# Kernel tuning notes

Measured on AMD Instinct MI355X. Metric: run time of the kernel, lower is better.

Reference implementation:

```python
import jax, jax.numpy as jnp
import numpy as np

N_NODES = 100000
N_EDGES = 1600000


def _spmm(row, col, val, x, n):
    # out[i] = sum_{e: row[e]==i} val[e] * x[col[e]]  (sparse adj @ dense x)
    return jax.ops.segment_sum(val[:, None] * x[col], row, num_segments=n)


def setup_inputs() -> dict:
    key = jax.random.key(0)
    ks = jax.random.split(key, 6)
    x = jax.random.normal(ks[0], (N_NODES, 128), dtype=jnp.float32)
    edge_row = jnp.sort(jax.random.randint(ks[1], (N_EDGES,), 0, N_NODES, dtype=jnp.int64))
    edge_col = jax.random.randint(ks[2], (N_EDGES,), 0, N_NODES, dtype=jnp.int64)
    # glorot-initialized linear layers (pyg Linear with weight_initializer='glorot')
    W0 = jax.random.normal(ks[3], (128, 128), dtype=jnp.float32) * np.sqrt(2.0 / (128 + 128))
    b0 = jnp.zeros((128,), dtype=jnp.float32)
    W1 = jax.random.normal(ks[4], (128, 64), dtype=jnp.float32) * np.sqrt(2.0 / (128 + 64))
    b1 = jnp.zeros((64,), dtype=jnp.float32)
    return {"x": x, "edge_row": edge_row, "edge_col": edge_col,
            "W0": W0, "b0": b0, "W1": W1, "b1": b1}


def reference(x, edge_row, edge_col, W0, b0, W1, b1):
    n = x.shape[0]
    # adj_norm: symmetric GCN normalization D^{-1/2} A D^{-1/2}
    ones = jnp.ones(edge_row.shape[0], dtype=x.dtype)
    deg = jax.ops.segment_sum(ones, edge_row, num_segments=n)
    dinv = jnp.where(deg > 0, jax.lax.rsqrt(jnp.maximum(deg, 1.0)), 0.0).astype(x.dtype)
    val = dinv[edge_row] * dinv[edge_col]
    # layer 0: linear -> SpMM -> relu (dropout is a no-op in inference/eval)
    h = x @ W0 + b0
    h = _spmm(edge_row, edge_col, val, h, n)
    h = jax.nn.relu(h)
    # layer 1: linear -> SpMM
    h = h @ W1 + b1
    h = _spmm(edge_row, edge_col, val, h, n)
    return jax.nn.log_softmax(h, axis=-1)
```

## Files before the change

kernel.cpp:

```cpp
#include <hip/hip_runtime.h>
#include <hip/hip_bf16.h>

#define NN 100000
#define NE 1600000

typedef __bf16 bf16x8 __attribute__((ext_vector_type(8)));
typedef float  f32x4  __attribute__((ext_vector_type(4)));

__global__ __launch_bounds__(256) void build_rowptr(const int* __restrict__ row,
                                                    int* __restrict__ row_ptr,
                                                    int E, int N) {
    int e = blockIdx.x * blockDim.x + threadIdx.x;
    if (e >= E) return;
    int r  = row[e];
    int rp = (e == 0) ? -1 : row[e - 1];
    for (int i = rp + 1; i <= r; ++i) row_ptr[i] = e;
    if (e == E - 1) {
        for (int i = r + 1; i <= N; ++i) row_ptr[i] = E;
    }
}

__global__ __launch_bounds__(256) void compute_dinv(const int* __restrict__ row_ptr,
                                                    float* __restrict__ dinv, int N) {
    int i = blockIdx.x * blockDim.x + threadIdx.x;
    if (i >= N) return;
    int deg = row_ptr[i + 1] - row_ptr[i];
    dinv[i] = (deg > 0) ? rsqrtf((float)deg) : 0.0f;
}

__global__ __launch_bounds__(256) void pack_weights(const float* __restrict__ W0,
                                                    const float* __restrict__ W1,
                                                    __hip_bfloat16* __restrict__ Wt0,
                                                    __hip_bfloat16* __restrict__ Wt1) {
    int idx = blockIdx.x * 256 + threadIdx.x;
    if (idx < 128 * 128) {
        int n = idx >> 7, k = idx & 127;
        Wt0[idx] = __float2bfloat16(W0[(size_t)k * 128 + n]);
    } else if (idx < 128 * 128 + 64 * 128) {
        int r = idx - 128 * 128;
        int n = r >> 7, k = r & 127;
        Wt1[r] = __float2bfloat16(W1[(size_t)k * 64 + n]);
    }
}

template <int NO, typename InT>
__global__ __launch_bounds__(512) void gemm_mfma(const InT* __restrict__ X,
                                                 const __hip_bfloat16* __restrict__ Wt,
                                                 const float* __restrict__ bias,
                                                 const float* __restrict__ rowscale,
                                                 __hip_bfloat16* __restrict__ out, int M) {
    constexpr int NT = NO / 16;
    __shared__ unsigned short As[128 * 128];
    __shared__ unsigned short Ws[NO * 128];

    const int t = threadIdx.x;
    const int w = t >> 6, lane = t & 63;
    const int l15 = lane & 15, quad = lane >> 4;
    const int rbase = blockIdx.x * 128;

    for (int i = t; i < NO * 16; i += 512) {
        int n = i >> 4, g = i & 15;
        *(uint4*)&Ws[n * 128 + ((g ^ (n & 7)) << 3)] = ((const uint4*)Wt)[i];
    }
    if constexpr (sizeof(InT) == 4) {
        for (int i = t; i < 4096; i += 512) {
            int r = i >> 5, c2 = i & 31;
            float4 xv = make_float4(0.f, 0.f, 0.f, 0.f);
            if (rbase + r < M) xv = ((const float4*)X)[(size_t)rbase * 32 + i];
            union { __hip_bfloat162 h; unsigned int u; } p0, p1;
            p0.h = __float22bfloat162_rn(make_float2(xv.x, xv.y));
            p1.h = __float22bfloat162_rn(make_float2(xv.z, xv.w));
            int phys = ((c2 >> 1) ^ (r & 7));
            *(uint2*)&As[r * 128 + (phys << 3) + ((c2 & 1) << 2)] = make_uint2(p0.u, p1.u);
        }
    } else {
        for (int i = t; i < 2048; i += 512) {
            int r = i >> 4, g = i & 15;
            uint4 v = make_uint4(0u, 0u, 0u, 0u);
            if (rbase + r < M) v = ((const uint4*)X)[(size_t)rbase * 16 + i];
            *(uint4*)&As[r * 128 + ((g ^ (r & 7)) << 3)] = v;
        }
    }
    __syncthreads();

    f32x4 acc[NT];
#pragma unroll
    for (int nt = 0; nt < NT; ++nt) {
        float bv = bias[nt * 16 + l15];
        acc[nt][0] = bv; acc[nt][1] = bv; acc[nt][2] = bv; acc[nt][3] = bv;
    }

    const int arow = w * 16 + l15;
    const int asw  = arow & 7;
#pragma unroll
    for (int kc = 0; kc < 4; ++kc) {
        bf16x8 af = *(const bf16x8*)&As[arow * 128 + (((kc * 4 + quad) ^ asw) << 3)];
#pragma unroll
        for (int nt = 0; nt < NT; ++nt) {
            int brow = nt * 16 + l15;
            bf16x8 bfr = *(const bf16x8*)&Ws[brow * 128 + (((kc * 4 + quad) ^ (brow & 7)) << 3)];
            acc[nt] = __builtin_amdgcn_mfma_f32_16x16x32_bf16(af, bfr, acc[nt], 0, 0, 0);
        }
    }

    __hip_bfloat16* Cs = (__hip_bfloat16*)As;
#pragma unroll
    for (int r4 = 0; r4 < 4; ++r4) {
        int lrow = w * 16 + quad * 4 + r4;
        int grow = rbase + lrow;
        float sc = (grow < M) ? rowscale[grow] : 0.f;
#pragma unroll
        for (int nt = 0; nt < NT; ++nt) {
            int ct = nt * 16 + l15;
            Cs[lrow * 128 + ((((ct >> 3) ^ (lrow & 7)) << 3)) + (ct & 7)] =
                __float2bfloat16(acc[nt][r4] * sc);
        }
    }
    constexpr int RJ  = NO / 8;
    constexpr int CNT = (16 * RJ) / 64;
#pragma unroll
    for (int k = 0; k < CNT; ++k) {
        int idx = k * 64 + lane;
        int lr16 = idx / RJ, j = idx % RJ;
        int lrow = w * 16 + lr16;
        int grow = rbase + lrow;
        if (grow < M) {
            uint4 v = *(const uint4*)&Cs[lrow * 128 + ((j ^ (lrow & 7)) << 3)];
            *(uint4*)&out[(size_t)grow * NO + (j << 3)] = v;
        }
    }
}

__global__ __launch_bounds__(256) void spmm_relu_128(const int* __restrict__ row_ptr,
                                                     const int* __restrict__ col,
                                                     const float* __restrict__ dinv,
                                                     const unsigned int* __restrict__ H,
                                                     __hip_bfloat16* __restrict__ out, int N) {
    const int lane = threadIdx.x & 63;
    int i = __builtin_amdgcn_readfirstlane(blockIdx.x * 4 + (threadIdx.x >> 6));
    if (i >= N) return;
    const float di = dinv[i];
    const int e0 = __builtin_amdgcn_readfirstlane(row_ptr[i]);
    const int e1 = __builtin_amdgcn_readfirstlane(row_ptr[i + 1]);
    float accx = 0.f, accy = 0.f;
    int e = e0;
    for (; e + 16 <= e1; e += 16) {
        unsigned int u[16];
#pragma unroll
        for (int j = 0; j < 16; ++j) {
            int c = __builtin_amdgcn_readfirstlane(col[e + j]);
            u[j] = H[(size_t)c * 64 + lane];
        }
#pragma unroll
        for (int j = 0; j < 16; ++j) {
            accx += __uint_as_float(u[j] << 16);
            accy += __uint_as_float(u[j] & 0xffff0000u);
        }
    }
    for (; e + 8 <= e1; e += 8) {
        unsigned int u[8];
#pragma unroll
        for (int j = 0; j < 8; ++j) {
            int c = __builtin_amdgcn_readfirstlane(col[e + j]);
            u[j] = H[(size_t)c * 64 + lane];
        }
#pragma unroll
        for (int j = 0; j < 8; ++j) {
            accx += __uint_as_float(u[j] << 16);
            accy += __uint_as_float(u[j] & 0xffff0000u);
        }
    }
    for (; e < e1; ++e) {
        int c = __builtin_amdgcn_readfirstlane(col[e]);
        unsigned int u = H[(size_t)c * 64 + lane];
        accx += __uint_as_float(u << 16);
        accy += __uint_as_float(u & 0xffff0000u);
    }
    accx = fmaxf(accx * di, 0.f);
    accy = fmaxf(accy * di, 0.f);
    *(__hip_bfloat162*)&out[(size_t)i * 128 + 2 * lane] =
        __float22bfloat162_rn(make_float2(accx, accy));
}

__global__ __launch_bounds__(256) void spmm_logsoftmax_64(const int* __restrict__ row_ptr,
                                                          const int* __restrict__ col,
                                                          const float* __restrict__ dinv,
                                                          const unsigned short* __restrict__ H,
                                                          float* __restrict__ out, int N) {
    const int lane = threadIdx.x & 63;
    int i = __builtin_amdgcn_readfirstlane(blockIdx.x * 4 + (threadIdx.x >> 6));
    if (i >= N) return;
    const float di = dinv[i];
    const int e0 = __builtin_amdgcn_readfirstlane(row_ptr[i]);
    const int e1 = __builtin_amdgcn_readfirstlane(row_ptr[i + 1]);
    float acc = 0.f;
    int e = e0;
    for (; e + 16 <= e1; e += 16) {
        unsigned short u[16];
#pragma unroll
        for (int j = 0; j < 16; ++j) {
            int c = __builtin_amdgcn_readfirstlane(col[e + j]);
            u[j] = H[(size_t)c * 64 + lane];
        }
#pragma unroll
        for (int j = 0; j < 16; ++j)
            acc += __uint_as_float((unsigned int)u[j] << 16);
    }
    for (; e + 8 <= e1; e += 8) {
        unsigned short u[8];
#pragma unroll
        for (int j = 0; j < 8; ++j) {
            int c = __builtin_amdgcn_readfirstlane(col[e + j]);
            u[j] = H[(size_t)c * 64 + lane];
        }
#pragma unroll
        for (int j = 0; j < 8; ++j)
            acc += __uint_as_float((unsigned int)u[j] << 16);
    }
    for (; e < e1; ++e) {
        int c = __builtin_amdgcn_readfirstlane(col[e]);
        acc += __uint_as_float((unsigned int)H[(size_t)c * 64 + lane] << 16);
    }
    acc *= di;
    float m = acc;
#pragma unroll
    for (int off = 32; off > 0; off >>= 1)
        m = fmaxf(m, __shfl_xor(m, off, 64));
    float ex = __expf(acc - m);
    float s = ex;
#pragma unroll
    for (int off = 32; off > 0; off >>= 1)
        s += __shfl_xor(s, off, 64);
    out[(size_t)i * 64 + lane] = acc - m - __logf(s);
}

extern "C" void kernel_launch(void* const* d_in, const int* in_sizes, int n_in,
                              void* d_out, int out_size, void* d_ws, size_t ws_size,
                              hipStream_t stream) {
    const float* x    = (const float*)d_in[0];
    const int*   erow = (const int*)d_in[1];
    const int*   ecol = (const int*)d_in[2];
    const float* W0   = (const float*)d_in[3];
    const float* b0   = (const float*)d_in[4];
    const float* W1   = (const float*)d_in[5];
    const float* b1   = (const float*)d_in[6];
    float* out = (float*)d_out;

    char* ws = (char*)d_ws;
    int*             row_ptr = (int*)ws;
    float*           dinv    = (float*)(ws + (512u << 10));
    __hip_bfloat16*  h0b     = (__hip_bfloat16*)(ws + (1u << 20));
    __hip_bfloat16*  h1b     = (__hip_bfloat16*)(ws + 27000000u);
    __hip_bfloat16*  h2b     = (__hip_bfloat16*)(ws + 53000000u);
    __hip_bfloat16*  Wt0     = (__hip_bfloat16*)(ws + 66000000u);
    __hip_bfloat16*  Wt1     = (__hip_bfloat16*)(ws + 66100000u);

    build_rowptr<<<(NE + 255) / 256, 256, 0, stream>>>(erow, row_ptr, NE, NN);
    compute_dinv<<<(NN + 255) / 256, 256, 0, stream>>>(row_ptr, dinv, NN);
    pack_weights<<<(128 * 128 + 64 * 128 + 255) / 256, 256, 0, stream>>>(W0, W1, Wt0, Wt1);

    gemm_mfma<128, float><<<(NN + 127) / 128, 512, 0, stream>>>(x, Wt0, b0, dinv, h0b, NN);
    spmm_relu_128<<<(NN + 3) / 4, 256, 0, stream>>>(row_ptr, ecol, dinv,
                                                    (const unsigned int*)h0b, h1b, NN);
    gemm_mfma<64, __hip_bfloat16><<<(NN + 127) / 128, 512, 0, stream>>>(h1b, Wt1, b1, dinv, h2b, NN);
    spmm_logsoftmax_64<<<(NN + 3) / 4, 256, 0, stream>>>(row_ptr, ecol, dinv,
                                                         (const unsigned short*)h2b, out, NN);
}
```

Baseline: 249.1 us.

## Merge prep kernels, compute degree scale inline, read weights from global in GEMM

Merges row-pointer construction and weight packing into one prep launch. It drops the separate dinv kernel and buffer, recomputing the degree scale from row_ptr inside the GEMM epilogue and the SpMM kernels. The GEMM no longer stages weights in shared memory; it loads B fragments directly from global (L2/L1 cached), and the k-loop is no longer unrolled. This cuts two launches and some LDS traffic, but adds redundant global weight loads per block and may serialize the MFMA loop.

Measured after the change: 273.3 us. 1.1x slower.

```diff
diff --git a/kernel.cpp b/kernel.cpp
--- a/kernel.cpp
+++ b/kernel.cpp
@@ -7,61 +7,53 @@
 typedef __bf16 bf16x8 __attribute__((ext_vector_type(8)));
 typedef float  f32x4  __attribute__((ext_vector_type(4)));
 
-__global__ __launch_bounds__(256) void build_rowptr(const int* __restrict__ row,
-                                                    int* __restrict__ row_ptr,
-                                                    int E, int N) {
-    int e = blockIdx.x * blockDim.x + threadIdx.x;
-    if (e >= E) return;
-    int r  = row[e];
-    int rp = (e == 0) ? -1 : row[e - 1];
-    for (int i = rp + 1; i <= r; ++i) row_ptr[i] = e;
-    if (e == E - 1) {
-        for (int i = r + 1; i <= N; ++i) row_ptr[i] = E;
-    }
-}
-
-__global__ __launch_bounds__(256) void compute_dinv(const int* __restrict__ row_ptr,
-                                                    float* __restrict__ dinv, int N) {
-    int i = blockIdx.x * blockDim.x + threadIdx.x;
-    if (i >= N) return;
-    int deg = row_ptr[i + 1] - row_ptr[i];
-    dinv[i] = (deg > 0) ? rsqrtf((float)deg) : 0.0f;
-}
-
-__global__ __launch_bounds__(256) void pack_weights(const float* __restrict__ W0,
-                                                    const float* __restrict__ W1,
-                                                    __hip_bfloat16* __restrict__ Wt0,
-                                                    __hip_bfloat16* __restrict__ Wt1) {
-    int idx = blockIdx.x * 256 + threadIdx.x;
-    if (idx < 128 * 128) {
-        int n = idx >> 7, k = idx & 127;
-        Wt0[idx] = __float2bfloat16(W0[(size_t)k * 128 + n]);
-    } else if (idx < 128 * 128 + 64 * 128) {
-        int r = idx - 128 * 128;
-        int n = r >> 7, k = r & 127;
-        Wt1[r] = __float2bfloat16(W1[(size_t)k * 64 + n]);
-    }
+__global__ __launch_bounds__(256) void prep_kernel(const int* __restrict__ row,
+                                                   int* __restrict__ row_ptr,
+                                                   const float* __restrict__ W0,
+                                                   const float* __restrict__ W1,
+                                                   __hip_bfloat16* __restrict__ Wt0,
+                                                   __hip_bfloat16* __restrict__ Wt1) {
+    int b = blockIdx.x;
+    if (b < NE / 256) {
+        int e = b * 256 + threadIdx.x;
+        int r  = row[e];
+        int rp = (e == 0) ? -1 : row[e - 1];
+        for (int i = rp + 1; i <= r; ++i) row_ptr[i] = e;
+        if (e == NE - 1) {
+            for (int i = r + 1; i <= NN; ++i) row_ptr[i] = NE;
+        }
+    } else {
+        int idx = (b - NE / 256) * 256 + threadIdx.x;
+        if (idx < 128 * 128) {
+            int n = idx >> 7, k = idx & 127;
+            Wt0[idx] = __float2bfloat16(W0[(size_t)k * 128 + n]);
+        } else {
+            int r2 = idx - 128 * 128;
+            int n = r2 >> 7, k = r2 & 127;
+            Wt1[r2] = __float2bfloat16(W1[(size_t)k * 64 + n]);
+        }
+    }
+}
+
+__device__ inline float deg_scale(const int* __restrict__ row_ptr, int i) {
+    int dg = row_ptr[i + 1] - row_ptr[i];
+    return (dg > 0) ? rsqrtf((float)dg) : 0.0f;
 }
 
 template <int NO, typename InT>
 __global__ __launch_bounds__(512) void gemm_mfma(const InT* __restrict__ X,
                                                  const __hip_bfloat16* __restrict__ Wt,
                                                  const float* __restrict__ bias,
-                                                 const float* __restrict__ rowscale,
+                                                 const int* __restrict__ row_ptr,
                                                  __hip_bfloat16* __restrict__ out, int M) {
     constexpr int NT = NO / 16;
     __shared__ unsigned short As[128 * 128];
-    __shared__ unsigned short Ws[NO * 128];
 
     const int t = threadIdx.x;
     const int w = t >> 6, lane = t & 63;
     const int l15 = lane & 15, quad = lane >> 4;
     const int rbase = blockIdx.x * 128;
 
-    for (int i = t; i < NO * 16; i += 512) {
-        int n = i >> 4, g = i & 15;
-        *(uint4*)&Ws[n * 128 + ((g ^ (n & 7)) << 3)] = ((const uint4*)Wt)[i];
-    }
     if constexpr (sizeof(InT) == 4) {
         for (int i = t; i < 4096; i += 512) {
             int r = i >> 5, c2 = i & 31;
@@ -92,13 +84,12 @@
 
     const int arow = w * 16 + l15;
     const int asw  = arow & 7;
-#pragma unroll
+#pragma unroll 1
     for (int kc = 0; kc < 4; ++kc) {
         bf16x8 af = *(const bf16x8*)&As[arow * 128 + (((kc * 4 + quad) ^ asw) << 3)];
 #pragma unroll
         for (int nt = 0; nt < NT; ++nt) {
-            int brow = nt * 16 + l15;
-            bf16x8 bfr = *(const bf16x8*)&Ws[brow * 128 + (((kc * 4 + quad) ^ (brow & 7)) << 3)];
+            bf16x8 bfr = *(const bf16x8*)&Wt[(size_t)(nt * 16 + l15) * 128 + kc * 32 + quad * 8];
             acc[nt] = __builtin_amdgcn_mfma_f32_16x16x32_bf16(af, bfr, acc[nt], 0, 0, 0);
         }
     }
@@ -108,7 +99,7 @@
     for (int r4 = 0; r4 < 4; ++r4) {
         int lrow = w * 16 + quad * 4 + r4;
         int grow = rbase + lrow;
-        float sc = (grow < M) ? rowscale[grow] : 0.f;
+        float sc = (grow < M) ? deg_scale(row_ptr, grow) : 0.f;
 #pragma unroll
         for (int nt = 0; nt < NT; ++nt) {
             int ct = nt * 16 + l15;
@@ -133,15 +124,15 @@
 
 __global__ __launch_bounds__(256) void spmm_relu_128(const int* __restrict__ row_ptr,
                                                      const int* __restrict__ col,
-                                                     const float* __restrict__ dinv,
                                                      const unsigned int* __restrict__ H,
                                                      __hip_bfloat16* __restrict__ out, int N) {
     const int lane = threadIdx.x & 63;
     int i = __builtin_amdgcn_readfirstlane(blockIdx.x * 4 + (threadIdx.x >> 6));
     if (i >= N) return;
-    const float di = dinv[i];
     const int e0 = __builtin_amdgcn_readfirstlane(row_ptr[i]);
     const int e1 = __builtin_amdgcn_readfirstlane(row_ptr[i + 1]);
+    const int dg = e1 - e0;
+    const float di = (dg > 0) ? rsqrtf((float)dg) : 0.0f;
     float accx = 0.f, accy = 0.f;
     int e = e0;
     for (; e + 16 <= e1; e += 16) {
@@ -184,15 +175,15 @@
 
 __global__ __launch_bounds__(256) void spmm_logsoftmax_64(const int* __restrict__ row_ptr,
                                                           const int* __restrict__ col,
-                                                          const float* __restrict__ dinv,
                                                           const unsigned short* __restrict__ H,
                                                           float* __restrict__ out, int N) {
     const int lane = threadIdx.x & 63;
     int i = __builtin_amdgcn_readfirstlane(blockIdx.x * 4 + (threadIdx.x >> 6));
     if (i >= N) return;
-    const float di = dinv[i];
     const int e0 = __builtin_amdgcn_readfirstlane(row_ptr[i]);
     const int e1 = __builtin_amdgcn_readfirstlane(row_ptr[i + 1]);
+    const int dg = e1 - e0;
+    const float di = (dg > 0) ? rsqrtf((float)dg) : 0.0f;
     float acc = 0.f;
     int e = e0;
     for (; e + 16 <= e1; e += 16) {
@@ -248,21 +239,17 @@
 
     char* ws = (char*)d_ws;
     int*             row_ptr = (int*)ws;
-    float*           dinv    = (float*)(ws + (512u << 10));
     __hip_bfloat16*  h0b     = (__hip_bfloat16*)(ws + (1u << 20));
     __hip_bfloat16*  h1b     = (__hip_bfloat16*)(ws + 27000000u);
     __hip_bfloat16*  h2b     = (__hip_bfloat16*)(ws + 53000000u);
     __hip_bfloat16*  Wt0     = (__hip_bfloat16*)(ws + 66000000u);
     __hip_bfloat16*  Wt1     = (__hip_bfloat16*)(ws + 66100000u);
 
-    build_rowptr<<<(NE + 255) / 256, 256, 0, stream>>>(erow, row_ptr, NE, NN);
-    compute_dinv<<<(NN + 255) / 256, 256, 0, stream>>>(row_ptr, dinv, NN);
-    pack_weights<<<(128 * 128 + 64 * 128 + 255) / 256, 256, 0, stream>>>(W0, W1, Wt0, Wt1);
-
-    gemm_mfma<128, float><<<(NN + 127) / 128, 512, 0, stream>>>(x, Wt0, b0, dinv, h0b, NN);
-    spmm_relu_128<<<(NN + 3) / 4, 256, 0, stream>>>(row_ptr, ecol, dinv,
+    prep_kernel<<<NE / 256 + 96, 256, 0, stream>>>(erow, row_ptr, W0, W1, Wt0, Wt1);
+    gemm_mfma<128, float><<<(NN + 127) / 128, 512, 0, stream>>>(x, Wt0, b0, row_ptr, h0b, NN);
+    spmm_relu_128<<<(NN + 3) / 4, 256, 0, stream>>>(row_ptr, ecol,
                                                     (const unsigned int*)h0b, h1b, NN);
-    gemm_mfma<64, __hip_bfloat16><<<(NN + 127) / 128, 512, 0, stream>>>(h1b, Wt1, b1, dinv, h2b, NN);
-    spmm_logsoftmax_64<<<(NN + 3) / 4, 256, 0, stream>>>(row_ptr, ecol, dinv,
+    gemm_mfma<64, __hip_bfloat16><<<(NN + 127) / 128, 512, 0, stream>>>(h1b, Wt1, b1, row_ptr, h2b, NN);
+    spmm_logsoftmax_64<<<(NN + 3) / 4, 256, 0, stream>>>(row_ptr, ecol,
                                                          (const unsigned short*)h2b, out, NN);
 }
```
